# Kernel optimization log

Hardware: AMD Instinct MI355X
Metric: run time of the kernel (lower is better)

The kernel has to match this reference:

```python
import jax, jax.numpy as jnp
import numpy as np

S = 192          # seq_len = h*w = 24*8
FF = 2048        # dim_feedforward
CH = [171, 171, 170]  # d_model=512 chunked over 3 layers
EPS = 1e-5


def _bn(x, axes):
    # training-mode BatchNorm with gamma=1, beta=0 (default init; xavier only touches dim>1 weights)
    m = x.mean(axis=axes, keepdims=True)
    v = x.var(axis=axes, keepdims=True)
    return (x - m) / jnp.sqrt(v + EPS)


def _layer(tgt, mem, fc1_w, fc1_b, se, fc2_w, fc2_b, fc3_w, fc3_b):
    # tgt: [q, s, d], mem: [k, s, d]
    q, s, d = tgt.shape
    k = mem.shape[0]
    qy = tgt @ fc1_w.T + fc1_b            # [q, s, d]
    ky = mem @ fc1_w.T + fc1_b            # [k, s, d]
    # correlation volume gated by learned sigmoid bias -> [q, k, s, t]
    vol = jnp.einsum('qtd,ksd->qkst', qy, ky) * jax.nn.sigmoid(se)
    sc = jnp.concatenate([vol.max(axis=2).reshape(q * k, s),   # max over s -> per-t
                          vol.max(axis=3).reshape(q * k, s)],  # max over t -> per-s
                         axis=-1)                               # [q*k, 2s]
    sc = _bn(sc.reshape(-1, 1, s), (0, 2)).reshape(-1, s)       # bn1 over (N, L)
    sc = jax.nn.relu(_bn(sc @ fc2_w.T + fc2_b, (0,)))           # fc2 + bn2 + relu
    sc = sc @ fc3_w.T + fc3_b                                   # [2*q*k, 1]
    sc = _bn(sc.reshape(-1, 2).sum(-1, keepdims=True), (0,))    # combine halves + bn3
    return sc.reshape(q, k)


def _forward(gallery, query, params):
    # gallery/query: NCHW -> [B, H, W, C]; tgt = gallery (memory in TransMatcher), memory arg = query
    g = jnp.transpose(gallery, (0, 2, 3, 1))
    f = jnp.transpose(query, (0, 2, 3, 1))
    q, k = g.shape[0], f.shape[0]
    g = g.reshape(q, S, -1)
    f = f.reshape(k, S, -1)
    start = 0
    score = jnp.zeros((q, k), dtype=g.dtype)
    for i, c in enumerate(CH):
        score = score + _layer(g[..., start:start + c], f[..., start:start + c], *params[i])
        start += c
    # decoder norm: BatchNorm1d(1) over flattened scores
    return _bn(score.reshape(-1, 1), (0,)).reshape(q, k)


def setup_inputs() -> dict:
    key = jax.random.key(0)
    ks = iter(jax.random.split(key, 32))
    d = {
        'gallery': jax.random.normal(next(ks), (32, 512, 24, 8), jnp.float32),
        'query': jax.random.normal(next(ks), (32, 512, 24, 8), jnp.float32),
    }
    def xavier(k, shape):
        fan_in, fan_out = shape[1], shape[0]
        lim = np.sqrt(6.0 / (fan_in + fan_out)).astype(np.float32)
        return jax.random.uniform(k, shape, jnp.float32, -lim, lim)
    for i, c in enumerate(CH):
        d[f'l{i}_fc1_w'] = xavier(next(ks), (c, c))
        d[f'l{i}_fc1_b'] = jax.random.normal(next(ks), (c,), jnp.float32) * 0.02
        d[f'l{i}_se'] = xavier(next(ks), (S, S))
        d[f'l{i}_fc2_w'] = xavier(next(ks), (FF, S))
        d[f'l{i}_fc2_b'] = jax.random.normal(next(ks), (FF,), jnp.float32) * 0.02
        d[f'l{i}_fc3_w'] = xavier(next(ks), (1, FF))
        d[f'l{i}_fc3_b'] = jax.random.normal(next(ks), (1,), jnp.float32) * 0.02
    return d


def reference(gallery, query,
              l0_fc1_w, l0_fc1_b, l0_se, l0_fc2_w, l0_fc2_b, l0_fc3_w, l0_fc3_b,
              l1_fc1_w, l1_fc1_b, l1_se, l1_fc2_w, l1_fc2_b, l1_fc3_w, l1_fc3_b,
              l2_fc1_w, l2_fc1_b, l2_se, l2_fc2_w, l2_fc2_b, l2_fc3_w, l2_fc3_b):
    params = [
        (l0_fc1_w, l0_fc1_b, l0_se, l0_fc2_w, l0_fc2_b, l0_fc3_w, l0_fc3_b),
        (l1_fc1_w, l1_fc1_b, l1_se, l1_fc2_w, l1_fc2_b, l1_fc3_w, l1_fc3_b),
        (l2_fc1_w, l2_fc1_b, l2_se, l2_fc2_w, l2_fc2_b, l2_fc3_w, l2_fc3_b),
    ]
    return _forward(gallery, query, params)
```

## Files before the change

kernel.cpp:

```cpp
#include <hip/hip_runtime.h>
#include <math.h>

#define EPS 1e-5f
#define TOTAL_IN (32*512*192)
#define CPAD 176
#define MPAD 192
#define KSTEPS 11
#define PACK_BK 6144

#define OFF_SIGSE 0u
#define OFF_W1T   110592u
#define OFF_QPACK 141568u
#define OFF_KPACK 1222912u
#define OFF_SC    2304256u
#define OFF_OUT2  2697472u
#define OFF_QSLAB OFF_OUT2
#define OFF_KSLAB (OFF_OUT2 + 1081344u)
#define OFF_COLP  6891776u
#define OFF_M2V2  7022848u
#define OFF_Y     7026944u
#define OFF_SCORE 7028992u

#define B_SIGSE 0u
#define B_W1T   110592u
#define B_SCPF  211968u
#define B_W2PF  1391616u
#define B_COLP  2571264u
#define B_M2R2  2767872u
#define B_Y     2780160u
#define B_SC3   2786304u
#define B_BIG   2789376u
#define B_SLAB  B_BIG
#define B_PACKF (B_BIG + 6488064u)
#define B_OUT2  B_BIG
#define B_TOTAL 15765504u

typedef __attribute__((ext_vector_type(8)))  short short8;
typedef __attribute__((ext_vector_type(16))) float f32x16;

__device__ __forceinline__ unsigned short f2bf(float x) {
    unsigned u = __float_as_uint(x);
    u += 0x7fffu + ((u >> 16) & 1u);
    return (unsigned short)(u >> 16);
}
__device__ __forceinline__ float bf2f(unsigned short h) {
    return __uint_as_float(((unsigned)h) << 16);
}

__device__ __forceinline__ void g2lds16(const void* g, void* l) {
    __builtin_amdgcn_global_load_lds((const __attribute__((address_space(1))) unsigned int*)g,
                                     (__attribute__((address_space(3))) unsigned int*)l, 16, 0, 0);
}

__global__ void k_sigse(const float* __restrict__ se0, const float* __restrict__ se1,
                        const float* __restrict__ se2, float* __restrict__ dst) {
    int idx = blockIdx.x * 256 + threadIdx.x;
    if (idx >= 3 * 36864) return;
    int l = idx / 36864, r = idx % 36864;
    const float* se = (l == 0) ? se0 : ((l == 1) ? se1 : se2);
    float x = se[r];
    dst[idx] = 1.0f / (1.0f + __expf(-x));
}


__global__ void k_w1t_b(const float* __restrict__ w1_0, const float* __restrict__ w1_1,
                        const float* __restrict__ w1_2, float* __restrict__ w1t) {
    int idx = blockIdx.x * 256 + threadIdx.x;
    if (idx >= 3 * CPAD * MPAD) return;
    int l = idx / (CPAD * MPAD), r = idx % (CPAD * MPAD);
    int i = r / MPAD, j = r % MPAD;
    int c = (l == 2) ? 170 : 171;
    const float* w1 = (l == 0) ? w1_0 : ((l == 1) ? w1_1 : w1_2);
    w1t[idx] = (i < c && j < c) ? w1[j * c + i] : 0.0f;
}

__global__ __launch_bounds__(256, 4)
void k_fc1_b(const float* __restrict__ g0, const float* __restrict__ g1,
             const float* __restrict__ w1tb,
             const float* __restrict__ b1_0, const float* __restrict__ b1_1,
             const float* __restrict__ b1_2, float* __restrict__ slabs) {
    __shared__ float As[2 * 16 * MPAD];
    __shared__ float Bs[2 * 16 * 64];
    const int quad = blockIdx.x, b = blockIdx.y, z = blockIdx.z;
    const int l = z >> 1, tensor = z & 1;
    const int c = (l == 2) ? 170 : 171, st = l * 171;
    const float* inp = tensor ? g1 : g0;
    const float* w1t = w1tb + (unsigned)l * (CPAD * MPAD);
    const float* b1 = (l == 0) ? b1_0 : ((l == 1) ? b1_1 : b1_2);
    float* dst = slabs + (size_t)z * 1081344u;
    const int tid = threadIdx.x, ty = tid >> 4, tx = tid & 15;
    const size_t boff = (size_t)b * 98304 + (size_t)st * 192 + (size_t)quad * 64;

    float acc[12][4];
#pragma unroll
    for (int i = 0; i < 12; ++i)
#pragma unroll
        for (int j = 0; j < 4; ++j) acc[i][j] = 0.0f;

    float4 v[4];
    auto load_chunk = [&](int ci) {
#pragma unroll
        for (int e = 0; e < 4; ++e) {
            int f = tid + (e << 8);
            if (f < 768) {
                v[e] = *(const float4*)(w1t + ci * 3072 + f * 4);
            } else {
                int f2 = f - 768;
                int r = f2 >> 4, c4 = f2 & 15;
                size_t off = boff + (size_t)(ci * 16 + r) * 192 + c4 * 4;
                if (off > (size_t)(TOTAL_IN - 4)) off = (size_t)(TOTAL_IN - 4);
                v[e] = *(const float4*)(inp + off);
            }
        }
    };
    auto write_chunk = [&](int buf) {
        float* Ad = As + buf * 3072;
        float* Bd = Bs + buf * 1024;
#pragma unroll
        for (int e = 0; e < 4; ++e) {
            int f = tid + (e << 8);
            if (f < 768) *(float4*)(Ad + f * 4) = v[e];
            else         *(float4*)(Bd + (f - 768) * 4) = v[e];
        }
    };

    load_chunk(0); write_chunk(0);
    __syncthreads();

    for (int ci = 0; ci < 11; ++ci) {
        const int buf = ci & 1;
        const bool pf = (ci + 1 < 11);
        if (pf) load_chunk(ci + 1);

        const float* Aw = As + buf * 3072 + ty * 12;
        const float* Bw = Bs + buf * 1024 + tx * 4;
#pragma unroll 2
        for (int kk = 0; kk < 16; ++kk) {
            const float4* ap = (const float4*)(Aw + kk * MPAD);
            float4 A0 = ap[0], A1 = ap[1], A2 = ap[2];
            float a[12] = {A0.x, A0.y, A0.z, A0.w, A1.x, A1.y, A1.z, A1.w, A2.x, A2.y, A2.z, A2.w};
            float4 B0 = *(const float4*)(Bw + kk * 64);
            float bb[4] = {B0.x, B0.y, B0.z, B0.w};
#pragma unroll
            for (int i = 0; i < 12; ++i)
#pragma unroll
                for (int j = 0; j < 4; ++j)
                    acc[i][j] = fmaf(a[i], bb[j], acc[i][j]);
        }
        if (pf) write_chunk(buf ^ 1);
        __syncthreads();
    }

    float* drow = dst + (size_t)b * (CPAD * 192) + quad * 64;
#pragma unroll
    for (int i = 0; i < 12; ++i) {
        int j = ty * 12 + i;
        if (j >= CPAD) continue;
        bool valid = (j < c);
        float bias = valid ? b1[j] : 0.0f;
        float o[4];
#pragma unroll
        for (int jj = 0; jj < 4; ++jj) o[jj] = valid ? (acc[i][jj] + bias) : 0.0f;
        *(float4*)(drow + (size_t)j * 192 + tx * 4) = make_float4(o[0], o[1], o[2], o[3]);
    }
}

__global__ void k_pack_b(const float* __restrict__ slabs, short* __restrict__ packs) {
    const int kstep = blockIdx.x, b = blockIdx.y, z = blockIdx.z;
    const float* src = slabs + (size_t)z * 1081344u + (size_t)b * (CPAD * 192);
    short* dst = packs + (size_t)z * 2162688u + (size_t)(b * KSTEPS + kstep) * PACK_BK;
    const int t = threadIdx.x;
    const int tile = t >> 6, lane = t & 63;
    const int hf = (lane >> 5) & 1, col = lane & 31;
    const int dbase = kstep * 16 + hf * 8;
    const int x = tile * 32 + col;

    short8 H, L;
#pragma unroll
    for (int e = 0; e < 8; ++e) {
        float v = src[(size_t)(dbase + e) * 192 + x];
        unsigned short h = f2bf(v);
        unsigned short l = f2bf(v - bf2f(h));
        H[e] = (short)h;
        L[e] = (short)l;
    }
    ((short8*)dst)[(0 * 6 + tile) * 64 + lane] = H;
    ((short8*)dst)[(1 * 6 + tile) * 64 + lane] = L;
}

__global__ void k_w2p(const float* __restrict__ w2_0, const float* __restrict__ w2_1,
                      const float* __restrict__ w2_2, short* __restrict__ w2p) {
    const int jt = blockIdx.x, l = blockIdx.y;
    const float* w2 = (l == 0) ? w2_0 : ((l == 1) ? w2_1 : w2_2);
    short* WP = w2p + (size_t)l * 786432u;
    const int tid = threadIdx.x, lane = tid & 63, sub = tid >> 6;
    const int j = jt * 32 + (lane & 31), hf = lane >> 5;
#pragma unroll
    for (int kk = 0; kk < 3; ++kk) {
        int ks = sub * 3 + kk;
        const float4* src = (const float4*)(w2 + (size_t)j * 192 + ks * 16 + hf * 8);
        float4 a = src[0], b = src[1];
        float v[8] = {a.x, a.y, a.z, a.w, b.x, b.y, b.z, b.w};
        short8 H, L;
#pragma unroll
        for (int e = 0; e < 8; ++e) {
            unsigned short h = f2bf(v[e]);
            H[e] = (short)h;
            L[e] = (short)f2bf(v[e] - bf2f(h));
        }
        ((short8*)WP)[((jt * 12 + ks) * 2 + 0) * 64 + lane] = H;
        ((short8*)WP)[((jt * 12 + ks) * 2 + 1) * 64 + lane] = L;
    }
}

__global__ __launch_bounds__(256, 2)
void k_corr_b(const short* __restrict__ packs, const float* __restrict__ sigb,
              short* __restrict__ scp) {
    __shared__ short smem[2 * 12288];
    const int qk = blockIdx.x, l = blockIdx.y;
    const int q = qk >> 5, k = qk & 31;
    const int tid = threadIdx.x, lane = tid & 63, w = tid >> 6;
    const int ws = w >> 1, wt = w & 1;
    const short* qpack = packs + (size_t)(l * 2 + 0) * 2162688u;
    const short* kpack = packs + (size_t)(l * 2 + 1) * 2162688u;
    const float* sig = sigb + (unsigned)l * 36864u;
    short* scpl = scp + (size_t)l * 786432u;
    const char* Abase = (const char*)(kpack + (size_t)k * KSTEPS * PACK_BK);
    const char* Bbase = (const char*)(qpack + (size_t)q * KSTEPS * PACK_BK);

    f32x16 acc[3][3];
#pragma unroll
    for (int i = 0; i < 3; ++i)
#pragma unroll
        for (int j = 0; j < 3; ++j)
#pragma unroll
            for (int r = 0; r < 16; ++r) acc[i][j][r] = 0.0f;

    auto stage = [&](int buf, int ks) {
#pragma unroll
        for (int u = 0; u < 6; ++u) {
            int c = u * 4 + w;
            const char* g = (c < 12 ? Abase + (size_t)ks * 12288 + c * 1024
                                    : Bbase + (size_t)ks * 12288 + (c - 12) * 1024) + lane * 16;
            g2lds16(g, (char*)smem + buf * 24576 + c * 1024);
        }
    };

    stage(0, 0);
    __syncthreads();

    int buf = 0;
    for (int ks = 0; ks < KSTEPS; ++ks) {
        if (ks + 1 < KSTEPS) stage(buf ^ 1, ks + 1);

        const short8* LA = (const short8*)((const char*)smem + buf * 24576);
        const short8* LB = (const short8*)((const char*)smem + buf * 24576 + 12288);
        short8 Ah[3], Al[3], Bh[3], Bl[3];
#pragma unroll
        for (int u = 0; u < 3; ++u) {
            Ah[u] = LA[(0 * 6 + ws * 3 + u) * 64 + lane];
            Al[u] = LA[(1 * 6 + ws * 3 + u) * 64 + lane];
            Bh[u] = LB[(0 * 6 + wt * 3 + u) * 64 + lane];
            Bl[u] = LB[(1 * 6 + wt * 3 + u) * 64 + lane];
        }
#pragma unroll
        for (int i = 0; i < 3; ++i)
#pragma unroll
            for (int j = 0; j < 3; ++j) {
                acc[i][j] = __builtin_amdgcn_mfma_f32_32x32x16_bf16(Ah[i], Bh[j], acc[i][j], 0, 0, 0);
                acc[i][j] = __builtin_amdgcn_mfma_f32_32x32x16_bf16(Al[i], Bh[j], acc[i][j], 0, 0, 0);
                acc[i][j] = __builtin_amdgcn_mfma_f32_32x32x16_bf16(Ah[i], Bl[j], acc[i][j], 0, 0, 0);
            }
        __syncthreads();
        buf ^= 1;
    }

    const int col = lane & 31, hf = lane >> 5;
    float* scr = (float*)smem;
    float cm[3] = {-3.0e38f, -3.0e38f, -3.0e38f};
#pragma unroll
    for (int i = 0; i < 3; ++i) {
        const int sbase = (ws * 3 + i) * 32;
        float rv[16];
#pragma unroll
        for (int r = 0; r < 16; ++r) rv[r] = -3.0e38f;
#pragma unroll
        for (int j = 0; j < 3; ++j) {
            const int tb = (wt * 3 + j) * 32 + col;
#pragma unroll
            for (int r = 0; r < 16; ++r) {
                int row = (r & 3) + 8 * (r >> 2) + 4 * hf;
                float v = acc[i][j][r] * sig[(size_t)(sbase + row) * 192 + tb];
                rv[r] = fmaxf(rv[r], v);
                cm[j] = fmaxf(cm[j], v);
            }
        }
#pragma unroll
        for (int m = 1; m < 32; m <<= 1)
#pragma unroll
            for (int r = 0; r < 16; ++r) rv[r] = fmaxf(rv[r], __shfl_xor(rv[r], m));
#pragma unroll
        for (int r = 0; r < 16; ++r)
            if (col == r)
                scr[384 + wt * 192 + sbase + (r & 3) + 8 * (r >> 2) + 4 * hf] = rv[r];
    }
#pragma unroll
    for (int j = 0; j < 3; ++j) {
        float c2 = fmaxf(cm[j], __shfl_xor(cm[j], 32));
        if (hf == 0) scr[ws * 192 + (wt * 3 + j) * 32 + col] = c2;
    }
    __syncthreads();
    if (tid < 96) {
        const int row = tid / 48, rem = tid % 48;
        const int ks2 = rem >> 2, hf2 = (rem >> 1) & 1, pl = rem & 1;
        const int r = 2 * qk + row;
        const float* s0 = scr + row * 384;
        short8 o;
#pragma unroll
        for (int e = 0; e < 8; ++e) {
            int t = ks2 * 16 + hf2 * 8 + e;
            float v = fmaxf(s0[t], s0[192 + t]);
            unsigned short h = f2bf(v);
            o[e] = pl ? (short)f2bf(v - bf2f(h)) : (short)h;
        }
        ((short8*)scpl)[(((r >> 5) * 12 + ks2) * 2 + pl) * 64 + (hf2 * 32 + (r & 31))] = o;
    }
}

__global__ __launch_bounds__(256, 2)
void k_fc2m_b(const short* __restrict__ scp, const short* __restrict__ w2p,
              float* __restrict__ out2b, float* __restrict__ colpb) {
    __shared__ short smem[2 * 8192];
    const int rblk = blockIdx.x & 15, nblk = blockIdx.x >> 4, l = blockIdx.y;
    float* out2 = out2b + (size_t)l * 4194304u;
    float* colp = colpb + (size_t)l * 65536u;
    const int tid = threadIdx.x, lane = tid & 63, w = tid >> 6;
    const int wr = w >> 1, wc = w & 1;
    const char* SPb = (const char*)(scp + (size_t)l * 786432u + (size_t)rblk * 4 * 12288u);
    const char* WPb = (const char*)(w2p + (size_t)l * 786432u + (size_t)nblk * 4 * 12288u);

    f32x16 acc[2][2];
#pragma unroll
    for (int i = 0; i < 2; ++i)
#pragma unroll
        for (int j = 0; j < 2; ++j)
#pragma unroll
            for (int r = 0; r < 16; ++r) acc[i][j][r] = 0.0f;

    auto stage = [&](int buf, int ks) {
#pragma unroll
        for (int u = 0; u < 4; ++u) {
            int c = u * 4 + w;
            const char* g = (c < 8 ? SPb + (c >> 1) * 24576 + ks * 2048 + (c & 1) * 1024
                                   : WPb + ((c - 8) >> 1) * 24576 + ks * 2048 + (c & 1) * 1024) + lane * 16;
            g2lds16(g, (char*)smem + buf * 16384 + c * 1024);
        }
    };

    stage(0, 0);
    __syncthreads();

    int buf = 0;
    for (int ks = 0; ks < 12; ++ks) {
        if (ks + 1 < 12) stage(buf ^ 1, ks + 1);

        const char* base = (const char*)smem + buf * 16384;
        short8 Ah[2], Al[2], Bh[2], Bl[2];
#pragma unroll
        for (int mt = 0; mt < 2; ++mt) {
            Ah[mt] = *(const short8*)(base + ((wr * 2 + mt) * 2 + 0) * 1024 + lane * 16);
            Al[mt] = *(const short8*)(base + ((wr * 2 + mt) * 2 + 1) * 1024 + lane * 16);
        }
#pragma unroll
        for (int nt = 0; nt < 2; ++nt) {
            Bh[nt] = *(const short8*)(base + 8192 + ((wc * 2 + nt) * 2 + 0) * 1024 + lane * 16);
            Bl[nt] = *(const short8*)(base + 8192 + ((wc * 2 + nt) * 2 + 1) * 1024 + lane * 16);
        }
#pragma unroll
        for (int mt = 0; mt < 2; ++mt)
#pragma unroll
            for (int nt = 0; nt < 2; ++nt) {
                acc[mt][nt] = __builtin_amdgcn_mfma_f32_32x32x16_bf16(Ah[mt], Bh[nt], acc[mt][nt], 0, 0, 0);
                acc[mt][nt] = __builtin_amdgcn_mfma_f32_32x32x16_bf16(Al[mt], Bh[nt], acc[mt][nt], 0, 0, 0);
                acc[mt][nt] = __builtin_amdgcn_mfma_f32_32x32x16_bf16(Ah[mt], Bl[nt], acc[mt][nt], 0, 0, 0);
            }
        __syncthreads();
        buf ^= 1;
    }

    const int hf = lane >> 5, cl = lane & 31;
#pragma unroll
    for (int mt = 0; mt < 2; ++mt)
#pragma unroll
        for (int nt = 0; nt < 2; ++nt) {
            const int c0 = nblk * 128 + (wc * 2 + nt) * 32 + cl;
#pragma unroll
            for (int r = 0; r < 16; ++r) {
                int row = rblk * 128 + (wr * 2 + mt) * 32 + (r & 3) + 8 * (r >> 2) + 4 * hf;
                out2[(size_t)row * 2048 + c0] = acc[mt][nt][r];
            }
        }
    float* cs = (float*)smem;
    float* cq = cs + 512;
#pragma unroll
    for (int nt = 0; nt < 2; ++nt) {
        float s = 0.0f, q2 = 0.0f;
#pragma unroll
        for (int mt = 0; mt < 2; ++mt)
#pragma unroll
            for (int r = 0; r < 16; ++r) { float v = acc[mt][nt][r]; s += v; q2 += v * v; }
        int ci = (wc * 2 + nt) * 32 + cl;
        cs[ci * 4 + wr * 2 + hf] = s;
        cq[ci * 4 + wr * 2 + hf] = q2;
    }
    __syncthreads();
    if (tid < 128) {
        float s = 0.0f, q2 = 0.0f;
#pragma unroll
        for (int u = 0; u < 4; ++u) { s += cs[tid * 4 + u]; q2 += cq[tid * 4 + u]; }
        colp[((size_t)rblk * 2048 + nblk * 128 + tid) * 2 + 0] = s;
        colp[((size_t)rblk * 2048 + nblk * 128 + tid) * 2 + 1] = q2;
    }
}

__global__ void k_colf_b(const float* __restrict__ colpb, float* __restrict__ m2r2b) {
    const int idx = blockIdx.x * 256 + threadIdx.x;
    if (idx >= 3 * 2048) return;
    const int l = idx >> 11, j = idx & 2047;
    const float* colp = colpb + (size_t)l * 65536u;
    float s = 0.0f, s2 = 0.0f;
    for (int bm = 0; bm < 16; ++bm) {
        s  += colp[((size_t)bm * 2048 + j) * 2 + 0];
        s2 += colp[((size_t)bm * 2048 + j) * 2 + 1];
    }
    float m = s * (1.0f / 2048.0f);
    float var = s2 * (1.0f / 2048.0f) - m * m;
    m2r2b[(size_t)l * 4096 + j * 2 + 0] = m;
    m2r2b[(size_t)l * 4096 + j * 2 + 1] = rsqrtf(var + EPS);
}

__global__ void k_fc3_b(const float* __restrict__ out2b, const float* __restrict__ m2r2b,
                        const float* __restrict__ w3_0, const float* __restrict__ w3_1,
                        const float* __restrict__ w3_2, float* __restrict__ yb) {
    const int rr = blockIdx.x, l = blockIdx.y;
    const float* out2 = out2b + (size_t)l * 4194304u;
    const float* m2r2 = m2r2b + (size_t)l * 4096u;
    const float* w3 = (l == 0) ? w3_0 : ((l == 1) ? w3_1 : w3_2);
    const int tid = threadIdx.x;
    __shared__ float red[4];
    float s = 0.0f;
    for (int j = tid; j < 2048; j += 256) {
        float2 mr = ((const float2*)m2r2)[j];
        float vv = (out2[(size_t)rr * 2048 + j] - mr.x) * mr.y;
        vv = fmaxf(vv, 0.0f);
        s += vv * w3[j];
    }
#pragma unroll
    for (int off = 32; off; off >>= 1) s += __shfl_xor(s, off);
    if ((tid & 63) == 0) red[tid >> 6] = s;
    __syncthreads();
    if (tid == 0) yb[(size_t)l * 2048 + rr] = red[0] + red[1] + red[2] + red[3];
}

__global__ void k_bn3_b(const float* __restrict__ yb, float* __restrict__ sc3) {
    const int l = blockIdx.x, tid = threadIdx.x;
    const float* y = yb + (size_t)l * 2048u;
    __shared__ float rs[4], rs2[4];
    float p[4]; float s = 0.0f, s2 = 0.0f;
#pragma unroll
    for (int u = 0; u < 4; ++u) {
        int i = tid + (u << 8);
        float vv = y[2 * i] + y[2 * i + 1];
        p[u] = vv; s += vv; s2 += vv * vv;
    }
#pragma unroll
    for (int off = 32; off; off >>= 1) { s += __shfl_xor(s, off); s2 += __shfl_xor(s2, off); }
    if ((tid & 63) == 0) { rs[tid >> 6] = s; rs2[tid >> 6] = s2; }
    __syncthreads();
    float S = rs[0] + rs[1] + rs[2] + rs[3];
    float S2 = rs2[0] + rs2[1] + rs2[2] + rs2[3];
    float m = S * (1.0f / 1024.0f);
    float var = S2 * (1.0f / 1024.0f) - m * m;
    float rstd = rsqrtf(var + EPS);
#pragma unroll
    for (int u = 0; u < 4; ++u) {
        int i = tid + (u << 8);
        sc3[(size_t)l * 1024 + i] = (p[u] - m) * rstd;
    }
}

__global__ void k_final3(const float* __restrict__ sc3, float* __restrict__ out) {
    const int tid = threadIdx.x;
    __shared__ float rs[4], rs2[4];
    float p[4]; float s = 0.0f, s2 = 0.0f;
#pragma unroll
    for (int u = 0; u < 4; ++u) {
        int i = tid + (u << 8);
        float vv = sc3[i] + sc3[1024 + i] + sc3[2048 + i];
        p[u] = vv; s += vv; s2 += vv * vv;
    }
#pragma unroll
    for (int off = 32; off; off >>= 1) { s += __shfl_xor(s, off); s2 += __shfl_xor(s2, off); }
    if ((tid & 63) == 0) { rs[tid >> 6] = s; rs2[tid >> 6] = s2; }
    __syncthreads();
    float S = rs[0] + rs[1] + rs[2] + rs[3];
    float S2 = rs2[0] + rs2[1] + rs2[2] + rs2[3];
    float m = S * (1.0f / 1024.0f);
    float var = S2 * (1.0f / 1024.0f) - m * m;
    float rstd = rsqrtf(var + EPS);
#pragma unroll
    for (int u = 0; u < 4; ++u) {
        int i = tid + (u << 8);
        out[i] = (p[u] - m) * rstd;
    }
}


__global__ void k_w1t(const float* __restrict__ w1, int c, float* __restrict__ w1t) {
    int idx = blockIdx.x * 256 + threadIdx.x;
    if (idx >= CPAD * CPAD) return;
    int i = idx / CPAD, j = idx % CPAD;
    w1t[idx] = (i < c && j < c) ? w1[j * c + i] : 0.0f;
}

__global__ __launch_bounds__(256, 4)
void k_fc1(const float* __restrict__ g0, const float* __restrict__ g1,
           const float* __restrict__ w1t, const float* __restrict__ b1,
           int c, int st, float* __restrict__ d0, float* __restrict__ d1) {
    __shared__ float As[2 * 16 * CPAD];
    __shared__ float Bs[2 * 16 * 64];
    const int quad = blockIdx.x, b = blockIdx.y, tensor = blockIdx.z;
    const float* inp = tensor ? g1 : g0;
    float* dst = tensor ? d1 : d0;
    const int tid = threadIdx.x, ty = tid >> 4, tx = tid & 15;
    const size_t boff = (size_t)b * 98304 + (size_t)st * 192 + (size_t)quad * 64;

    float acc[11][4];
#pragma unroll
    for (int i = 0; i < 11; ++i)
#pragma unroll
        for (int j = 0; j < 4; ++j) acc[i][j] = 0.0f;

    float4 v[4];
    auto load_chunk = [&](int ci) {
#pragma unroll
        for (int e = 0; e < 4; ++e) {
            int f = tid + (e << 8);
            if (f < 704) {
                v[e] = *(const float4*)(w1t + ci * 2816 + f * 4);
            } else if (f < 960) {
                int f2 = f - 704;
                int r = f2 >> 4, c4 = f2 & 15;
                size_t off = boff + (size_t)(ci * 16 + r) * 192 + c4 * 4;
                if (off > (size_t)(TOTAL_IN - 4)) off = (size_t)(TOTAL_IN - 4);
                v[e] = *(const float4*)(inp + off);
            }
        }
    };
    auto write_chunk = [&](int buf) {
        float* Ad = As + buf * 2816;
        float* Bd = Bs + buf * 1024;
#pragma unroll
        for (int e = 0; e < 4; ++e) {
            int f = tid + (e << 8);
            if (f < 704)      *(float4*)(Ad + f * 4) = v[e];
            else if (f < 960) *(float4*)(Bd + (f - 704) * 4) = v[e];
        }
    };

    load_chunk(0); write_chunk(0);
    __syncthreads();

    for (int ci = 0; ci < 11; ++ci) {
        const int buf = ci & 1;
        const bool pf = (ci + 1 < 11);
        if (pf) load_chunk(ci + 1);

        const float* Aw = As + buf * 2816 + ty * 11;
        const float* Bw = Bs + buf * 1024 + tx * 4;
#pragma unroll 2
        for (int kk = 0; kk < 16; ++kk) {
            float a[11];
#pragma unroll
            for (int i = 0; i < 11; ++i) a[i] = Aw[kk * CPAD + i];
            float4 B0 = *(const float4*)(Bw + kk * 64);
            float bb[4] = {B0.x, B0.y, B0.z, B0.w};
#pragma unroll
            for (int i = 0; i < 11; ++i)
#pragma unroll
                for (int j = 0; j < 4; ++j)
                    acc[i][j] = fmaf(a[i], bb[j], acc[i][j]);
        }
        if (pf) write_chunk(buf ^ 1);
        __syncthreads();
    }

    float* drow = dst + (size_t)b * (CPAD * 192) + quad * 64;
#pragma unroll
    for (int i = 0; i < 11; ++i) {
        int j = ty * 11 + i;
        bool valid = (j < c);
        float bias = valid ? b1[j] : 0.0f;
        float o[4];
#pragma unroll
        for (int jj = 0; jj < 4; ++jj) o[jj] = valid ? (acc[i][jj] + bias) : 0.0f;
        *(float4*)(drow + (size_t)j * 192 + tx * 4) = make_float4(o[0], o[1], o[2], o[3]);
    }
}

__global__ void k_pack(const float* __restrict__ qslab, const float* __restrict__ kslab,
                       short* __restrict__ qpack, short* __restrict__ kpack) {
    const int kstep = blockIdx.x, b = blockIdx.y, tensor = blockIdx.z;
    const float* src = (tensor ? kslab : qslab) + (size_t)b * (CPAD * 192);
    short* dst = (tensor ? kpack : qpack) + (size_t)(b * KSTEPS + kstep) * PACK_BK;
    const int t = threadIdx.x;
    const int tile = t >> 6, lane = t & 63;
    const int hf = (lane >> 5) & 1, col = lane & 31;
    const int dbase = kstep * 16 + hf * 8;
    const int x = tile * 32 + col;

    short8 H, L;
#pragma unroll
    for (int e = 0; e < 8; ++e) {
        float v = src[(size_t)(dbase + e) * 192 + x];
        unsigned short h = f2bf(v);
        unsigned short l = f2bf(v - bf2f(h));
        H[e] = (short)h;
        L[e] = (short)l;
    }
    ((short8*)dst)[(0 * 6 + tile) * 64 + lane] = H;
    ((short8*)dst)[(1 * 6 + tile) * 64 + lane] = L;
}

__global__ __launch_bounds__(256, 2)
void k_corr(const short* __restrict__ qpack, const short* __restrict__ kpack,
            const float* __restrict__ sig, float* __restrict__ sc) {
    __shared__ short smem[2 * 12288];
    const int qk = blockIdx.x, q = qk >> 5, k = qk & 31;
    const int tid = threadIdx.x, lane = tid & 63, w = tid >> 6;
    const int ws = w >> 1, wt = w & 1;
    const char* Abase = (const char*)(kpack + (size_t)k * KSTEPS * PACK_BK);
    const char* Bbase = (const char*)(qpack + (size_t)q * KSTEPS * PACK_BK);

    f32x16 acc[3][3];
#pragma unroll
    for (int i = 0; i < 3; ++i)
#pragma unroll
        for (int j = 0; j < 3; ++j)
#pragma unroll
            for (int r = 0; r < 16; ++r) acc[i][j][r] = 0.0f;

    auto stage = [&](int buf, int ks) {
#pragma unroll
        for (int u = 0; u < 6; ++u) {
            int c = u * 4 + w;
            const char* g = (c < 12 ? Abase + (size_t)ks * 12288 + c * 1024
                                    : Bbase + (size_t)ks * 12288 + (c - 12) * 1024) + lane * 16;
            g2lds16(g, (char*)smem + buf * 24576 + c * 1024);
        }
    };

    stage(0, 0);
    __syncthreads();

    int buf = 0;
    for (int ks = 0; ks < KSTEPS; ++ks) {
        if (ks + 1 < KSTEPS) stage(buf ^ 1, ks + 1);

        const short8* LA = (const short8*)((const char*)smem + buf * 24576);
        const short8* LB = (const short8*)((const char*)smem + buf * 24576 + 12288);
        short8 Ah[3], Al[3], Bh[3], Bl[3];
#pragma unroll
        for (int u = 0; u < 3; ++u) {
            Ah[u] = LA[(0 * 6 + ws * 3 + u) * 64 + lane];
            Al[u] = LA[(1 * 6 + ws * 3 + u) * 64 + lane];
            Bh[u] = LB[(0 * 6 + wt * 3 + u) * 64 + lane];
            Bl[u] = LB[(1 * 6 + wt * 3 + u) * 64 + lane];
        }
#pragma unroll
        for (int i = 0; i < 3; ++i)
#pragma unroll
            for (int j = 0; j < 3; ++j) {
                acc[i][j] = __builtin_amdgcn_mfma_f32_32x32x16_bf16(Ah[i], Bh[j], acc[i][j], 0, 0, 0);
                acc[i][j] = __builtin_amdgcn_mfma_f32_32x32x16_bf16(Al[i], Bh[j], acc[i][j], 0, 0, 0);
                acc[i][j] = __builtin_amdgcn_mfma_f32_32x32x16_bf16(Ah[i], Bl[j], acc[i][j], 0, 0, 0);
            }
        __syncthreads();
        buf ^= 1;
    }

    const int col = lane & 31, hf = lane >> 5;
    float* scr = (float*)smem;
    float cm[3] = {-3.0e38f, -3.0e38f, -3.0e38f};
#pragma unroll
    for (int i = 0; i < 3; ++i) {
        const int sbase = (ws * 3 + i) * 32;
        float rv[16];
#pragma unroll
        for (int r = 0; r < 16; ++r) rv[r] = -3.0e38f;
#pragma unroll
        for (int j = 0; j < 3; ++j) {
            const int tb = (wt * 3 + j) * 32 + col;
#pragma unroll
            for (int r = 0; r < 16; ++r) {
                int row = (r & 3) + 8 * (r >> 2) + 4 * hf;
                float v = acc[i][j][r] * sig[(size_t)(sbase + row) * 192 + tb];
                rv[r] = fmaxf(rv[r], v);
                cm[j] = fmaxf(cm[j], v);
            }
        }
#pragma unroll
        for (int m = 1; m < 32; m <<= 1)
#pragma unroll
            for (int r = 0; r < 16; ++r) rv[r] = fmaxf(rv[r], __shfl_xor(rv[r], m));
#pragma unroll
        for (int r = 0; r < 16; ++r)
            if (col == r)
                scr[384 + wt * 192 + sbase + (r & 3) + 8 * (r >> 2) + 4 * hf] = rv[r];
    }
#pragma unroll
    for (int j = 0; j < 3; ++j) {
        float c2 = fmaxf(cm[j], __shfl_xor(cm[j], 32));
        if (hf == 0) scr[ws * 192 + (wt * 3 + j) * 32 + col] = c2;
    }
    __syncthreads();
    if (tid < 192) {
        sc[(size_t)(2 * qk) * 192 + tid]     = fmaxf(scr[tid], scr[192 + tid]);
        sc[(size_t)(2 * qk + 1) * 192 + tid] = fmaxf(scr[384 + tid], scr[384 + 192 + tid]);
    }
}

__global__ __launch_bounds__(256, 2)
void k_fc2(const float* __restrict__ sc, const float* __restrict__ w2, float* __restrict__ out2) {
    __shared__ float Ast[32 * 132];
    __shared__ float Bst[32 * 132];
    const int bm = blockIdx.x & 15, bn = blockIdx.x >> 4;
    const int r0 = bm * 128, c0 = bn * 128;
    const int tid = threadIdx.x, ty = tid >> 4, tx = tid & 15;
    const int r = tid >> 1, half = (tid & 1) * 16;

    float acc[8][8];
#pragma unroll
    for (int i = 0; i < 8; ++i)
#pragma unroll
        for (int j = 0; j < 8; ++j) acc[i][j] = 0.0f;

    for (int t0 = 0; t0 < 192; t0 += 32) {
        float4 av[4], bv[4];
        const float4* ga = (const float4*)(sc + (size_t)(r0 + r) * 192 + t0 + half);
        const float4* gb = (const float4*)(w2 + (size_t)(c0 + r) * 192 + t0 + half);
#pragma unroll
        for (int e = 0; e < 4; ++e) { av[e] = ga[e]; bv[e] = gb[e]; }
        __syncthreads();
#pragma unroll
        for (int e = 0; e < 4; ++e) {
            int t = half + 4 * e;
            Ast[(t + 0) * 132 + r] = av[e].x;  Bst[(t + 0) * 132 + r] = bv[e].x;
            Ast[(t + 1) * 132 + r] = av[e].y;  Bst[(t + 1) * 132 + r] = bv[e].y;
            Ast[(t + 2) * 132 + r] = av[e].z;  Bst[(t + 2) * 132 + r] = bv[e].z;
            Ast[(t + 3) * 132 + r] = av[e].w;  Bst[(t + 3) * 132 + r] = bv[e].w;
        }
        __syncthreads();
#pragma unroll 4
        for (int kk = 0; kk < 32; ++kk) {
            const float4* ap = (const float4*)(Ast + kk * 132 + ty * 8);
            const float4* bp = (const float4*)(Bst + kk * 132 + tx * 8);
            float4 A0 = ap[0], A1 = ap[1];
            float4 B0 = bp[0], B1 = bp[1];
            float a[8] = {A0.x, A0.y, A0.z, A0.w, A1.x, A1.y, A1.z, A1.w};
            float b[8] = {B0.x, B0.y, B0.z, B0.w, B1.x, B1.y, B1.z, B1.w};
#pragma unroll
            for (int i = 0; i < 8; ++i)
#pragma unroll
                for (int j = 0; j < 8; ++j)
                    acc[i][j] = fmaf(a[i], b[j], acc[i][j]);
        }
    }
#pragma unroll
    for (int i = 0; i < 8; ++i) {
        float4* op = (float4*)(out2 + (size_t)(r0 + ty * 8 + i) * 2048 + c0 + tx * 8);
        op[0] = make_float4(acc[i][0], acc[i][1], acc[i][2], acc[i][3]);
        op[1] = make_float4(acc[i][4], acc[i][5], acc[i][6], acc[i][7]);
    }
}

__global__ void k_colp(const float* __restrict__ out2, float* __restrict__ colp) {
    const int bc = blockIdx.x & 7, br = blockIdx.x >> 3;
    const int j = bc * 256 + threadIdx.x;
    float s = 0.0f, s2 = 0.0f;
    for (int rr = br * 64; rr < br * 64 + 64; ++rr) {
        float vv = out2[(size_t)rr * 2048 + j];
        s += vv; s2 += vv * vv;
    }
    colp[((size_t)br * 2048 + j) * 2 + 0] = s;
    colp[((size_t)br * 2048 + j) * 2 + 1] = s2;
}

__global__ void k_colf(const float* __restrict__ colp, float* __restrict__ m2r2) {
    const int j = blockIdx.x * 256 + threadIdx.x;
    if (j >= 2048) return;
    float s = 0.0f, s2 = 0.0f;
    for (int br = 0; br < 32; ++br) {
        s  += colp[((size_t)br * 2048 + j) * 2 + 0];
        s2 += colp[((size_t)br * 2048 + j) * 2 + 1];
    }
    float m = s * (1.0f / 2048.0f);
    float var = s2 * (1.0f / 2048.0f) - m * m;
    m2r2[j * 2 + 0] = m;
    m2r2[j * 2 + 1] = rsqrtf(var + EPS);
}

__global__ void k_fc3(const float* __restrict__ out2, const float* __restrict__ m2r2,
                      const float* __restrict__ w3, float* __restrict__ y) {
    const int rr = blockIdx.x;
    const int tid = threadIdx.x;
    __shared__ float red[4];
    float s = 0.0f;
    for (int j = tid; j < 2048; j += 256) {
        float2 mr = ((const float2*)m2r2)[j];
        float vv = (out2[(size_t)rr * 2048 + j] - mr.x) * mr.y;
        vv = fmaxf(vv, 0.0f);
        s += vv * w3[j];
    }
#pragma unroll
    for (int off = 32; off; off >>= 1) s += __shfl_xor(s, off);
    if ((tid & 63) == 0) red[tid >> 6] = s;
    __syncthreads();
    if (tid == 0) y[rr] = red[0] + red[1] + red[2] + red[3];
}

__global__ void k_bn3(const float* __restrict__ y, float* __restrict__ score, int first) {
    const int tid = threadIdx.x;
    __shared__ float rs[4], rs2[4];
    float p[4]; float s = 0.0f, s2 = 0.0f;
#pragma unroll
    for (int u = 0; u < 4; ++u) {
        int i = tid + (u << 8);
        float vv = y[2 * i] + y[2 * i + 1];
        p[u] = vv; s += vv; s2 += vv * vv;
    }
#pragma unroll
    for (int off = 32; off; off >>= 1) { s += __shfl_xor(s, off); s2 += __shfl_xor(s2, off); }
    if ((tid & 63) == 0) { rs[tid >> 6] = s; rs2[tid >> 6] = s2; }
    __syncthreads();
    float S = rs[0] + rs[1] + rs[2] + rs[3];
    float S2 = rs2[0] + rs2[1] + rs2[2] + rs2[3];
    float m = S * (1.0f / 1024.0f);
    float var = S2 * (1.0f / 1024.0f) - m * m;
    float rstd = rsqrtf(var + EPS);
#pragma unroll
    for (int u = 0; u < 4; ++u) {
        int i = tid + (u << 8);
        float vv = (p[u] - m) * rstd;
        score[i] = first ? vv : (score[i] + vv);
    }
}

__global__ void k_final(const float* __restrict__ score, float* __restrict__ out) {
    const int tid = threadIdx.x;
    __shared__ float rs[4], rs2[4];
    float p[4]; float s = 0.0f, s2 = 0.0f;
#pragma unroll
    for (int u = 0; u < 4; ++u) {
        int i = tid + (u << 8);
        float vv = score[i];
        p[u] = vv; s += vv; s2 += vv * vv;
    }
#pragma unroll
    for (int off = 32; off; off >>= 1) { s += __shfl_xor(s, off); s2 += __shfl_xor(s2, off); }
    if ((tid & 63) == 0) { rs[tid >> 6] = s; rs2[tid >> 6] = s2; }
    __syncthreads();
    float S = rs[0] + rs[1] + rs[2] + rs[3];
    float S2 = rs2[0] + rs2[1] + rs2[2] + rs2[3];
    float m = S * (1.0f / 1024.0f);
    float var = S2 * (1.0f / 1024.0f) - m * m;
    float rstd = rsqrtf(var + EPS);
#pragma unroll
    for (int u = 0; u < 4; ++u) {
        int i = tid + (u << 8);
        out[i] = (p[u] - m) * rstd;
    }
}

extern "C" void kernel_launch(void* const* d_in, const int* in_sizes, int n_in,
                              void* d_out, int out_size, void* d_ws, size_t ws_size,
                              hipStream_t stream) {
    const float* gallery = (const float*)d_in[0];
    const float* query   = (const float*)d_in[1];
    float* ws = (float*)d_ws;

    const bool batched = (ws_size >= (size_t)B_TOTAL * sizeof(float));

    if (batched) {
        short* scp = (short*)(ws + B_SCPF);
        short* w2p = (short*)(ws + B_W2PF);

        k_sigse<<<(3 * 36864 + 255) / 256, 256, 0, stream>>>(
            (const float*)d_in[2 + 0 * 7 + 2], (const float*)d_in[2 + 1 * 7 + 2],
            (const float*)d_in[2 + 2 * 7 + 2], ws + B_SIGSE);
        k_w1t_b<<<(3 * CPAD * MPAD + 255) / 256, 256, 0, stream>>>(
            (const float*)d_in[2 + 0 * 7 + 0], (const float*)d_in[2 + 1 * 7 + 0],
            (const float*)d_in[2 + 2 * 7 + 0], ws + B_W1T);
        k_fc1_b<<<dim3(3, 32, 6), 256, 0, stream>>>(
            gallery, query, ws + B_W1T,
            (const float*)d_in[2 + 0 * 7 + 1], (const float*)d_in[2 + 1 * 7 + 1],
            (const float*)d_in[2 + 2 * 7 + 1], ws + B_SLAB);
        k_pack_b<<<dim3(KSTEPS, 32, 6), 384, 0, stream>>>(ws + B_SLAB, (short*)(ws + B_PACKF));
        k_w2p<<<dim3(64, 3), 256, 0, stream>>>(
            (const float*)d_in[2 + 0 * 7 + 3], (const float*)d_in[2 + 1 * 7 + 3],
            (const float*)d_in[2 + 2 * 7 + 3], w2p);
        k_corr_b<<<dim3(1024, 3), 256, 0, stream>>>((const short*)(ws + B_PACKF),
                                                    ws + B_SIGSE, scp);
        k_fc2m_b<<<dim3(256, 3), 256, 0, stream>>>(scp, w2p, ws + B_OUT2, ws + B_COLP);
        k_colf_b<<<24, 256, 0, stream>>>(ws + B_COLP, ws + B_M2R2);
        k_fc3_b<<<dim3(2048, 3), 256, 0, stream>>>(
            ws + B_OUT2, ws + B_M2R2,
            (const float*)d_in[2 + 0 * 7 + 5], (const float*)d_in[2 + 1 * 7 + 5],
            (const float*)d_in[2 + 2 * 7 + 5], ws + B_Y);
        k_bn3_b<<<3, 256, 0, stream>>>(ws + B_Y, ws + B_SC3);
        k_final3<<<1, 256, 0, stream>>>(ws + B_SC3, (float*)d_out);
        return;
    }

    const int cs[3] = {171, 171, 170};
    const int st[3] = {0, 171, 342};

    short* qpack = (short*)(ws + OFF_QPACK);
    short* kpack = (short*)(ws + OFF_KPACK);

    k_sigse<<<(3 * 36864 + 255) / 256, 256, 0, stream>>>(
        (const float*)d_in[2 + 0 * 7 + 2], (const float*)d_in[2 + 1 * 7 + 2],
        (const float*)d_in[2 + 2 * 7 + 2], ws + OFF_SIGSE);

    for (int l = 0; l < 3; ++l) {
        const float* w1 = (const float*)d_in[2 + l * 7 + 0];
        const float* b1 = (const float*)d_in[2 + l * 7 + 1];
        const float* w2 = (const float*)d_in[2 + l * 7 + 3];
        const float* w3 = (const float*)d_in[2 + l * 7 + 5];

        k_w1t<<<(CPAD * CPAD + 255) / 256, 256, 0, stream>>>(w1, cs[l], ws + OFF_W1T);
        k_fc1<<<dim3(3, 32, 2), 256, 0, stream>>>(gallery, query, ws + OFF_W1T, b1,
                                                  cs[l], st[l], ws + OFF_QSLAB, ws + OFF_KSLAB);
        k_pack<<<dim3(KSTEPS, 32, 2), 384, 0, stream>>>(ws + OFF_QSLAB, ws + OFF_KSLAB,
                                                        qpack, kpack);
        k_corr<<<1024, 256, 0, stream>>>(qpack, kpack, ws + OFF_SIGSE + l * 36864, ws + OFF_SC);
        k_fc2<<<256, 256, 0, stream>>>(ws + OFF_SC, w2, ws + OFF_OUT2);
        k_colp<<<256, 256, 0, stream>>>(ws + OFF_OUT2, ws + OFF_COLP);
        k_colf<<<8, 256, 0, stream>>>(ws + OFF_COLP, ws + OFF_M2V2);
        k_fc3<<<2048, 256, 0, stream>>>(ws + OFF_OUT2, ws + OFF_M2V2, w3, ws + OFF_Y);
        k_bn3<<<1, 256, 0, stream>>>(ws + OFF_Y, ws + OFF_SCORE, l == 0 ? 1 : 0);
    }
    k_final<<<1, 256, 0, stream>>>(ws + OFF_SCORE, (float*)d_out);
}
```

Before: 373.2 us.

## Fuse bf16 hi/lo packing into fc1 epilogue and swizzle corr block order

The fc1 GEMM now writes its results through shared memory and emits the split bf16 hi/lo packed layout directly. This removes the intermediate fp32 slab round-trip and the separate pack kernel launch. The correlation kernel also gets a flat 1D grid with an XCD-style swizzle, so blocks sharing the same layer and q/k land on the same chiplet for better L2 reuse. The fused epilogue adds extra syncthreads and reuses the 32KB smem in fc1.

```diff
diff --git a/kernel.cpp b/kernel.cpp
--- a/kernel.cpp
+++ b/kernel.cpp
@@ -30,7 +30,6 @@
 #define B_Y     2780160u
 #define B_SC3   2786304u
 #define B_BIG   2789376u
-#define B_SLAB  B_BIG
 #define B_PACKF (B_BIG + 6488064u)
 #define B_OUT2  B_BIG
 #define B_TOTAL 15765504u
@@ -75,20 +74,22 @@
 }
 
 __global__ __launch_bounds__(256, 4)
-void k_fc1_b(const float* __restrict__ g0, const float* __restrict__ g1,
-             const float* __restrict__ w1tb,
-             const float* __restrict__ b1_0, const float* __restrict__ b1_1,
-             const float* __restrict__ b1_2, float* __restrict__ slabs) {
-    __shared__ float As[2 * 16 * MPAD];
-    __shared__ float Bs[2 * 16 * 64];
+void k_fc1p_b(const float* __restrict__ g0, const float* __restrict__ g1,
+              const float* __restrict__ w1tb,
+              const float* __restrict__ b1_0, const float* __restrict__ b1_1,
+              const float* __restrict__ b1_2, short* __restrict__ packs) {
+    __shared__ float smem[8192];
+    float* As = smem;
+    float* Bs = smem + 6144;
     const int quad = blockIdx.x, b = blockIdx.y, z = blockIdx.z;
-    const int l = z >> 1, tensor = z & 1;
+    const int l = z >> 1;
     const int c = (l == 2) ? 170 : 171, st = l * 171;
-    const float* inp = tensor ? g1 : g0;
+    const float* inp = (z & 1) ? g1 : g0;
     const float* w1t = w1tb + (unsigned)l * (CPAD * MPAD);
     const float* b1 = (l == 0) ? b1_0 : ((l == 1) ? b1_1 : b1_2);
-    float* dst = slabs + (size_t)z * 1081344u;
+    short* dstb = packs + (size_t)z * 2162688u + (size_t)b * (KSTEPS * PACK_BK);
     const int tid = threadIdx.x, ty = tid >> 4, tx = tid & 15;
+    const int lane = tid & 63, w = tid >> 6;
     const size_t boff = (size_t)b * 98304 + (size_t)st * 192 + (size_t)quad * 64;
 
     float acc[12][4];
@@ -151,41 +152,38 @@
         __syncthreads();
     }
 
-    float* drow = dst + (size_t)b * (CPAD * 192) + quad * 64;
-#pragma unroll
-    for (int i = 0; i < 12; ++i) {
-        int j = ty * 12 + i;
-        if (j >= CPAD) continue;
-        bool valid = (j < c);
-        float bias = valid ? b1[j] : 0.0f;
-        float o[4];
-#pragma unroll
-        for (int jj = 0; jj < 4; ++jj) o[jj] = valid ? (acc[i][jj] + bias) : 0.0f;
-        *(float4*)(drow + (size_t)j * 192 + tx * 4) = make_float4(o[0], o[1], o[2], o[3]);
-    }
-}
-
-__global__ void k_pack_b(const float* __restrict__ slabs, short* __restrict__ packs) {
-    const int kstep = blockIdx.x, b = blockIdx.y, z = blockIdx.z;
-    const float* src = slabs + (size_t)z * 1081344u + (size_t)b * (CPAD * 192);
-    short* dst = packs + (size_t)z * 2162688u + (size_t)(b * KSTEPS + kstep) * PACK_BK;
-    const int t = threadIdx.x;
-    const int tile = t >> 6, lane = t & 63;
-    const int hf = (lane >> 5) & 1, col = lane & 31;
-    const int dbase = kstep * 16 + hf * 8;
-    const int x = tile * 32 + col;
-
-    short8 H, L;
-#pragma unroll
-    for (int e = 0; e < 8; ++e) {
-        float v = src[(size_t)(dbase + e) * 192 + x];
-        unsigned short h = f2bf(v);
-        unsigned short l = f2bf(v - bf2f(h));
-        H[e] = (short)h;
-        L[e] = (short)l;
-    }
-    ((short8*)dst)[(0 * 6 + tile) * 64 + lane] = H;
-    ((short8*)dst)[(1 * 6 + tile) * 64 + lane] = L;
+    const int hf = lane >> 5, col = lane & 31;
+#pragma unroll
+    for (int h = 0; h < 2; ++h) {
+        __syncthreads();
+        if ((tx >> 3) == h) {
+            const int tc = (tx & 7) * 4;
+#pragma unroll
+            for (int i = 0; i < 12; ++i) {
+                int j = ty * 12 + i;
+                bool valid = (j < c);
+                float bias = valid ? b1[j] : 0.0f;
+#pragma unroll
+                for (int jj = 0; jj < 4; ++jj)
+                    smem[j * 33 + tc + jj] = valid ? (acc[i][jj] + bias) : 0.0f;
+            }
+        }
+        __syncthreads();
+        const int tile = quad * 2 + h;
+        for (int ks = w; ks < KSTEPS; ks += 4) {
+            short8 H, L;
+#pragma unroll
+            for (int e = 0; e < 8; ++e) {
+                float vv = smem[(ks * 16 + hf * 8 + e) * 33 + col];
+                unsigned short hh = f2bf(vv);
+                H[e] = (short)hh;
+                L[e] = (short)f2bf(vv - bf2f(hh));
+            }
+            short8* dst = (short8*)(dstb + (size_t)ks * PACK_BK);
+            dst[(0 * 6 + tile) * 64 + lane] = H;
+            dst[(1 * 6 + tile) * 64 + lane] = L;
+        }
+    }
 }
 
 __global__ void k_w2p(const float* __restrict__ w2_0, const float* __restrict__ w2_1,
@@ -217,7 +215,9 @@
 void k_corr_b(const short* __restrict__ packs, const float* __restrict__ sigb,
               short* __restrict__ scp) {
     __shared__ short smem[2 * 12288];
-    const int qk = blockIdx.x, l = blockIdx.y;
+    const int orig = blockIdx.x;
+    const int swz = (orig & 7) * 384 + (orig >> 3);
+    const int l = swz >> 10, qk = swz & 1023;
     const int q = qk >> 5, k = qk & 31;
     const int tid = threadIdx.x, lane = tid & 63, w = tid >> 6;
     const int ws = w >> 1, wt = w & 1;
@@ -894,6 +894,7 @@
     if (batched) {
         short* scp = (short*)(ws + B_SCPF);
         short* w2p = (short*)(ws + B_W2PF);
+        short* packs = (short*)(ws + B_PACKF);
 
         k_sigse<<<(3 * 36864 + 255) / 256, 256, 0, stream>>>(
             (const float*)d_in[2 + 0 * 7 + 2], (const float*)d_in[2 + 1 * 7 + 2],
@@ -901,16 +902,14 @@
         k_w1t_b<<<(3 * CPAD * MPAD + 255) / 256, 256, 0, stream>>>(
             (const float*)d_in[2 + 0 * 7 + 0], (const float*)d_in[2 + 1 * 7 + 0],
             (const float*)d_in[2 + 2 * 7 + 0], ws + B_W1T);
-        k_fc1_b<<<dim3(3, 32, 6), 256, 0, stream>>>(
+        k_fc1p_b<<<dim3(3, 32, 6), 256, 0, stream>>>(
             gallery, query, ws + B_W1T,
             (const float*)d_in[2 + 0 * 7 + 1], (const float*)d_in[2 + 1 * 7 + 1],
-            (const float*)d_in[2 + 2 * 7 + 1], ws + B_SLAB);
-        k_pack_b<<<dim3(KSTEPS, 32, 6), 384, 0, stream>>>(ws + B_SLAB, (short*)(ws + B_PACKF));
+            (const float*)d_in[2 + 2 * 7 + 1], packs);
         k_w2p<<<dim3(64, 3), 256, 0, stream>>>(
             (const float*)d_in[2 + 0 * 7 + 3], (const float*)d_in[2 + 1 * 7 + 3],
             (const float*)d_in[2 + 2 * 7 + 3], w2p);
-        k_corr_b<<<dim3(1024, 3), 256, 0, stream>>>((const short*)(ws + B_PACKF),
-                                                    ws + B_SIGSE, scp);
+        k_corr_b<<<3072, 256, 0, stream>>>(packs, ws + B_SIGSE, scp);
         k_fc2m_b<<<dim3(256, 3), 256, 0, stream>>>(scp, w2p, ws + B_OUT2, ws + B_COLP);
         k_colf_b<<<24, 256, 0, stream>>>(ws + B_COLP, ws + B_M2R2);
         k_fc3_b<<<dim3(2048, 3), 256, 0, stream>>>(
```

After: 337.3 us. -9.6%, faster.
